# Kernel tuning notes

Measured on AMD Instinct MI355X. Metric: run time of the kernel, lower is better.

The kernel has to match this reference:

```python
import jax, jax.numpy as jnp
import numpy as np

EPS = 1e-9


def setup_inputs() -> dict:
    key = jax.random.key(0)
    k1, k2, k3, k4 = jax.random.split(key, 4)
    B, D, U = 1024, 512, 512
    x = jax.random.normal(k1, (B, D), dtype=jnp.float32)
    w = jax.random.normal(k2, (D, U), dtype=jnp.float32)
    p = jax.random.normal(k3, (D, U), dtype=jnp.float32)
    b = jax.random.normal(k4, (U,), dtype=jnp.float32)
    return {"x": x, "w": w, "p": p, "b": b}


def reference(x, w, p, b):
    # x: [B, D]; w, p: [D, U]; b: [U]
    xe = x[..., None] + EPS                      # [B, D, 1]
    abs_pow = jnp.abs(xe) ** p                   # [B, D, U]
    is_neg = xe < 0                              # [B, D, 1]
    odd_mask = jnp.mod(p, 2) != 0                # [D, U]
    signed = jnp.where(odd_mask & is_neg, -abs_pow, abs_pow)
    z = jnp.sum(w * signed, axis=1) + b          # [B, U]
    return z  # linear activation
```

## Files before the change

kernel.cpp:

```cpp
#include <hip/hip_runtime.h>
#include <math.h>

#define EPS 1e-9f

constexpr int Bn = 1024, Dn = 512, Un = 512;
constexpr int BM = 64;
constexpr int BU = 64;
constexpr int DK = 32;
constexpr int SPLITD = 8;
constexpr int DPB = Dn / SPLITD;
constexpr int NCHUNK = DPB / DK;

template <bool USE_WS>
__global__ __launch_bounds__(256, 4) void power_layer(
    const float* __restrict__ x, const float* __restrict__ w,
    const float* __restrict__ p, const float* __restrict__ bias,
    float* __restrict__ outp)
{
    __shared__ float sL[DK][BM];
    __shared__ float sP[DK][BU];
    __shared__ float sW[DK][BU];
    __shared__ float sWX[DK][BU];

    const int tid = threadIdx.x;
    const int tx  = tid & 15;
    const int ty  = tid >> 4;
    const int tx4 = tx * 4;
    const int ty4 = ty * 4;
    const int ub = blockIdx.x * BU;
    const int bb = blockIdx.y * BM;
    const int d0 = blockIdx.z * DPB;

    float acc[4][4] = {};

    for (int ch = 0; ch < NCHUNK; ++ch) {
        const int db = d0 + ch * DK;

        {
            int t = tid;
            #pragma unroll
            for (int it = 0; it < 2; ++it, t += 256) {
                const int r  = t >> 3;
                const int dq = (t & 7) << 2;
                const float4 xv = *reinterpret_cast<const float4*>(
                    &x[(size_t)(bb + r) * Dn + db + dq]);
                const float* xs = reinterpret_cast<const float*>(&xv);
                #pragma unroll
                for (int j = 0; j < 4; ++j) {
                    const float xe = xs[j] + EPS;
                    const float La = __builtin_amdgcn_logf(fabsf(xe)) + 64.0f;
                    sL[dq + j][r] = (xe < 0.0f) ? -La : La;
                }
            }
        }
        {
            int t = tid;
            #pragma unroll
            for (int it = 0; it < 2; ++it, t += 256) {
                const int d  = t >> 4;
                const int uq = (t & 15) << 2;
                const size_t gi = (size_t)(db + d) * Un + ub + uq;
                const float4 pv = *reinterpret_cast<const float4*>(&p[gi]);
                const float4 wv = *reinterpret_cast<const float4*>(&w[gi]);
                const float* ps  = reinterpret_cast<const float*>(&pv);
                const float* wsv = reinterpret_cast<const float*>(&wv);
                float4 wxv;
                float* wxs = reinterpret_cast<float*>(&wxv);
                #pragma unroll
                for (int j = 0; j < 4; ++j) {
                    const bool odd = (fmodf(ps[j], 2.0f) != 0.0f);
                    wxs[j] = odd ? -wsv[j] : wsv[j];
                }
                *reinterpret_cast<float4*>(&sP[d][uq])  = pv;
                *reinterpret_cast<float4*>(&sW[d][uq])  = wv;
                *reinterpret_cast<float4*>(&sWX[d][uq]) = wxv;
            }
        }
        __syncthreads();

        float4 Lv = *reinterpret_cast<const float4*>(&sL[0][ty4]);
        float4 Pv = *reinterpret_cast<const float4*>(&sP[0][tx4]);
        float4 Wv = *reinterpret_cast<const float4*>(&sW[0][tx4]);
        float4 Xv = *reinterpret_cast<const float4*>(&sWX[0][tx4]);

        #pragma unroll 4
        for (int d = 0; d < DK; ++d) {
            const int dn = (d + 1) & (DK - 1);
            const float4 Ln = *reinterpret_cast<const float4*>(&sL[dn][ty4]);
            const float4 Pn = *reinterpret_cast<const float4*>(&sP[dn][tx4]);
            const float4 Wn = *reinterpret_cast<const float4*>(&sW[dn][tx4]);
            const float4 Xn = *reinterpret_cast<const float4*>(&sWX[dn][tx4]);

            const float* Ls = reinterpret_cast<const float*>(&Lv);
            const float* Ps = reinterpret_cast<const float*>(&Pv);
            const float* Ws = reinterpret_cast<const float*>(&Wv);
            const float* Xs = reinterpret_cast<const float*>(&Xv);

            float Ld[4];
            bool  ng[4];
            #pragma unroll
            for (int r = 0; r < 4; ++r) {
                Ld[r] = fabsf(Ls[r]) - 64.0f;
                ng[r] = Ls[r] < 0.0f;
            }

            float ev[16];
            #pragma unroll
            for (int r = 0; r < 4; ++r)
                #pragma unroll
                for (int c = 0; c < 4; ++c)
                    ev[r * 4 + c] = __builtin_amdgcn_exp2f(Ps[c] * Ld[r]);

            #pragma unroll
            for (int r = 0; r < 4; ++r)
                #pragma unroll
                for (int c = 0; c < 4; ++c)
                    acc[r][c] = fmaf(ng[r] ? Xs[c] : Ws[c], ev[r * 4 + c], acc[r][c]);

            Lv = Ln; Pv = Pn; Wv = Wn; Xv = Xn;
        }
        __syncthreads();
    }

    if (USE_WS) {
        float* dst = outp + ((size_t)blockIdx.z * Bn + bb + ty4) * Un + ub + tx4;
        #pragma unroll
        for (int r = 0; r < 4; ++r) {
            float4 st = make_float4(acc[r][0], acc[r][1], acc[r][2], acc[r][3]);
            *reinterpret_cast<float4*>(dst + (size_t)r * Un) = st;
        }
    } else {
        if (blockIdx.z == 0) {
            const float4 bv = *reinterpret_cast<const float4*>(&bias[ub + tx4]);
            const float* bs = reinterpret_cast<const float*>(&bv);
            #pragma unroll
            for (int r = 0; r < 4; ++r)
                #pragma unroll
                for (int c = 0; c < 4; ++c)
                    acc[r][c] += bs[c];
        }
        #pragma unroll
        for (int r = 0; r < 4; ++r) {
            const int row = bb + ty4 + r;
            #pragma unroll
            for (int c = 0; c < 4; ++c)
                atomicAdd(&outp[(size_t)row * Un + ub + tx4 + c], acc[r][c]);
        }
    }
}

__global__ __launch_bounds__(256) void reduce_ws(
    const float* __restrict__ ws, const float* __restrict__ bias,
    float* __restrict__ out)
{
    const int nf4 = (Bn * Un) / 4;
    const int i = blockIdx.x * 256 + threadIdx.x;
    if (i >= nf4) return;
    const float4* w4 = reinterpret_cast<const float4*>(ws);
    float4 a = w4[i];
    #pragma unroll
    for (int z = 1; z < SPLITD; ++z) {
        const float4 t = w4[(size_t)z * nf4 + i];
        a.x += t.x; a.y += t.y; a.z += t.z; a.w += t.w;
    }
    const float4 bv = reinterpret_cast<const float4*>(bias)[i & (Un / 4 - 1)];
    a.x += bv.x; a.y += bv.y; a.z += bv.z; a.w += bv.w;
    reinterpret_cast<float4*>(out)[i] = a;
}

extern "C" void kernel_launch(void* const* d_in, const int* in_sizes, int n_in,
                              void* d_out, int out_size, void* d_ws, size_t ws_size,
                              hipStream_t stream) {
    const float* x = (const float*)d_in[0];
    const float* w = (const float*)d_in[1];
    const float* p = (const float*)d_in[2];
    const float* b = (const float*)d_in[3];
    float* out = (float*)d_out;

    const dim3 grid(Un / BU, Bn / BM, SPLITD);
    const size_t need = (size_t)SPLITD * Bn * Un * sizeof(float);

    if (ws_size >= need) {
        float* wsf = (float*)d_ws;
        power_layer<true><<<grid, dim3(256), 0, stream>>>(x, w, p, b, wsf);
        reduce_ws<<<dim3((Bn * Un / 4 + 255) / 256), dim3(256), 0, stream>>>(wsf, b, out);
    } else {
        hipMemsetAsync(out, 0, (size_t)out_size * sizeof(float), stream);
        power_layer<false><<<grid, dim3(256), 0, stream>>>(x, w, p, b, out);
    }
}
```

Before: 113.6 us.

## Shrink tile to 32x64 with 2x4 microtile, halve DK, swizzle log tile in LDS

```diff
diff --git a/kernel.cpp b/kernel.cpp
--- a/kernel.cpp
+++ b/kernel.cpp
@@ -4,12 +4,14 @@
 #define EPS 1e-9f
 
 constexpr int Bn = 1024, Dn = 512, Un = 512;
-constexpr int BM = 64;
+constexpr int BM = 32;
 constexpr int BU = 64;
-constexpr int DK = 32;
+constexpr int DK = 16;
 constexpr int SPLITD = 8;
 constexpr int DPB = Dn / SPLITD;
 constexpr int NCHUNK = DPB / DK;
+
+__device__ __forceinline__ int swz(int d) { return ((d >> 2) & 3) << 3; }
 
 template <bool USE_WS>
 __global__ __launch_bounds__(256, 4) void power_layer(
@@ -26,106 +28,90 @@
     const int tx  = tid & 15;
     const int ty  = tid >> 4;
     const int tx4 = tx * 4;
-    const int ty4 = ty * 4;
+    const int ty2 = ty * 2;
     const int ub = blockIdx.x * BU;
     const int bb = blockIdx.y * BM;
     const int d0 = blockIdx.z * DPB;
 
-    float acc[4][4] = {};
+    float acc[2][4] = {};
 
     for (int ch = 0; ch < NCHUNK; ++ch) {
         const int db = d0 + ch * DK;
 
-        {
-            int t = tid;
+        if (tid < 128) {
+            const int r  = tid >> 2;
+            const int dq = (tid & 3) << 2;
+            const float4 xv = *reinterpret_cast<const float4*>(
+                &x[(size_t)(bb + r) * Dn + db + dq]);
+            const float* xs = reinterpret_cast<const float*>(&xv);
             #pragma unroll
-            for (int it = 0; it < 2; ++it, t += 256) {
-                const int r  = t >> 3;
-                const int dq = (t & 7) << 2;
-                const float4 xv = *reinterpret_cast<const float4*>(
-                    &x[(size_t)(bb + r) * Dn + db + dq]);
-                const float* xs = reinterpret_cast<const float*>(&xv);
-                #pragma unroll
-                for (int j = 0; j < 4; ++j) {
-                    const float xe = xs[j] + EPS;
-                    const float La = __builtin_amdgcn_logf(fabsf(xe)) + 64.0f;
-                    sL[dq + j][r] = (xe < 0.0f) ? -La : La;
-                }
+            for (int j = 0; j < 4; ++j) {
+                const float xe = xs[j] + EPS;
+                const float La = __builtin_amdgcn_logf(fabsf(xe)) + 64.0f;
+                const int dd = dq + j;
+                sL[dd][r ^ swz(dd)] = (xe < 0.0f) ? -La : La;
             }
         }
         {
-            int t = tid;
+            const int d  = tid >> 4;
+            const int uq = (tid & 15) << 2;
+            const size_t gi = (size_t)(db + d) * Un + ub + uq;
+            const float4 pv = *reinterpret_cast<const float4*>(&p[gi]);
+            const float4 wv = *reinterpret_cast<const float4*>(&w[gi]);
+            const float* ps  = reinterpret_cast<const float*>(&pv);
+            const float* wsv = reinterpret_cast<const float*>(&wv);
+            float4 wxv;
+            float* wxs = reinterpret_cast<float*>(&wxv);
             #pragma unroll
-            for (int it = 0; it < 2; ++it, t += 256) {
-                const int d  = t >> 4;
-                const int uq = (t & 15) << 2;
-                const size_t gi = (size_t)(db + d) * Un + ub + uq;
-                const float4 pv = *reinterpret_cast<const float4*>(&p[gi]);
-                const float4 wv = *reinterpret_cast<const float4*>(&w[gi]);
-                const float* ps  = reinterpret_cast<const float*>(&pv);
-                const float* wsv = reinterpret_cast<const float*>(&wv);
-                float4 wxv;
-                float* wxs = reinterpret_cast<float*>(&wxv);
-                #pragma unroll
-                for (int j = 0; j < 4; ++j) {
-                    const bool odd = (fmodf(ps[j], 2.0f) != 0.0f);
-                    wxs[j] = odd ? -wsv[j] : wsv[j];
-                }
-                *reinterpret_cast<float4*>(&sP[d][uq])  = pv;
-                *reinterpret_cast<float4*>(&sW[d][uq])  = wv;
-                *reinterpret_cast<float4*>(&sWX[d][uq]) = wxv;
+            for (int j = 0; j < 4; ++j) {
+                const bool odd = (fmodf(ps[j], 2.0f) != 0.0f);
+                wxs[j] = odd ? -wsv[j] : wsv[j];
             }
+            *reinterpret_cast<float4*>(&sP[d][uq])  = pv;
+            *reinterpret_cast<float4*>(&sW[d][uq])  = wv;
+            *reinterpret_cast<float4*>(&sWX[d][uq]) = wxv;
         }
         __syncthreads();
 
-        float4 Lv = *reinterpret_cast<const float4*>(&sL[0][ty4]);
-        float4 Pv = *reinterpret_cast<const float4*>(&sP[0][tx4]);
-        float4 Wv = *reinterpret_cast<const float4*>(&sW[0][tx4]);
-        float4 Xv = *reinterpret_cast<const float4*>(&sWX[0][tx4]);
-
         #pragma unroll 4
         for (int d = 0; d < DK; ++d) {
-            const int dn = (d + 1) & (DK - 1);
-            const float4 Ln = *reinterpret_cast<const float4*>(&sL[dn][ty4]);
-            const float4 Pn = *reinterpret_cast<const float4*>(&sP[dn][tx4]);
-            const float4 Wn = *reinterpret_cast<const float4*>(&sW[dn][tx4]);
-            const float4 Xn = *reinterpret_cast<const float4*>(&sWX[dn][tx4]);
-
+            const float2 Lv = *reinterpret_cast<const float2*>(&sL[d][ty2 ^ swz(d)]);
+            const float4 Pv = *reinterpret_cast<const float4*>(&sP[d][tx4]);
+            const float4 Wv = *reinterpret_cast<const float4*>(&sW[d][tx4]);
+            const float4 Xv = *reinterpret_cast<const float4*>(&sWX[d][tx4]);
             const float* Ls = reinterpret_cast<const float*>(&Lv);
             const float* Ps = reinterpret_cast<const float*>(&Pv);
             const float* Ws = reinterpret_cast<const float*>(&Wv);
             const float* Xs = reinterpret_cast<const float*>(&Xv);
 
-            float Ld[4];
-            bool  ng[4];
+            float Ld[2];
+            bool  ng[2];
             #pragma unroll
-            for (int r = 0; r < 4; ++r) {
+            for (int r = 0; r < 2; ++r) {
                 Ld[r] = fabsf(Ls[r]) - 64.0f;
                 ng[r] = Ls[r] < 0.0f;
             }
 
-            float ev[16];
+            float ev[8];
             #pragma unroll
-            for (int r = 0; r < 4; ++r)
+            for (int r = 0; r < 2; ++r)
                 #pragma unroll
                 for (int c = 0; c < 4; ++c)
                     ev[r * 4 + c] = __builtin_amdgcn_exp2f(Ps[c] * Ld[r]);
 
             #pragma unroll
-            for (int r = 0; r < 4; ++r)
+            for (int r = 0; r < 2; ++r)
                 #pragma unroll
                 for (int c = 0; c < 4; ++c)
                     acc[r][c] = fmaf(ng[r] ? Xs[c] : Ws[c], ev[r * 4 + c], acc[r][c]);
-
-            Lv = Ln; Pv = Pn; Wv = Wn; Xv = Xn;
         }
         __syncthreads();
     }
 
     if (USE_WS) {
-        float* dst = outp + ((size_t)blockIdx.z * Bn + bb + ty4) * Un + ub + tx4;
+        float* dst = outp + ((size_t)blockIdx.z * Bn + bb + ty2) * Un + ub + tx4;
         #pragma unroll
-        for (int r = 0; r < 4; ++r) {
+        for (int r = 0; r < 2; ++r) {
             float4 st = make_float4(acc[r][0], acc[r][1], acc[r][2], acc[r][3]);
             *reinterpret_cast<float4*>(dst + (size_t)r * Un) = st;
         }
@@ -134,14 +120,14 @@
             const float4 bv = *reinterpret_cast<const float4*>(&bias[ub + tx4]);
             const float* bs = reinterpret_cast<const float*>(&bv);
             #pragma unroll
-            for (int r = 0; r < 4; ++r)
+            for (int r = 0; r < 2; ++r)
                 #pragma unroll
                 for (int c = 0; c < 4; ++c)
                     acc[r][c] += bs[c];
         }
         #pragma unroll
-        for (int r = 0; r < 4; ++r) {
-            const int row = bb + ty4 + r;
+        for (int r = 0; r < 2; ++r) {
+            const int row = bb + ty2 + r;
             #pragma unroll
             for (int c = 0; c < 4; ++c)
                 atomicAdd(&outp[(size_t)row * Un + ub + tx4 + c], acc[r][c]);
```

New measurement: 110.8 us. -2.5%, faster.
